# Kernel optimization log

Hardware: AMD Instinct MI355X
Metric: run time of the kernel (lower is better)

## Reference

```python
import jax, jax.numpy as jnp
import numpy as np


def setup_inputs() -> dict:
    key = jax.random.key(0)
    k1, k2 = jax.random.split(key)
    z_e_x = jax.random.normal(k1, (4096, 16, 128), dtype=jnp.float32)
    codebook = jax.random.normal(k2, (1024, 128), dtype=jnp.float32)
    return {"z_e_x": z_e_x, "codebook": codebook}


def reference(z_e_x, codebook):
    # VQStraightThrough.forward: nearest-codebook quantization in fp32.
    B, N, C = z_e_x.shape
    x = z_e_x.astype(jnp.float32).reshape(B * N, C)          # [BN, C]
    cb = codebook.astype(jnp.float32)                        # [K, C]
    inputs_sq = jnp.sum(x * x, axis=1, keepdims=True)        # [BN, 1]
    codebook_sq = jnp.sum(cb * cb, axis=1)                   # [K]
    l2_dis = inputs_sq + codebook_sq - 2.0 * (x @ cb.T)      # [BN, K]
    flat_idx = jnp.argmin(l2_dis, axis=1)                    # [BN] int
    min_vals = jnp.min(l2_dis, axis=1)                       # [BN]
    idx = flat_idx.reshape(B, N)
    distances = min_vals.reshape(B, N).astype(z_e_x.dtype)
    codes = cb[flat_idx].reshape(B, N, C).astype(z_e_x.dtype)  # gather
    return codes, flat_idx, idx, distances
```

## Files before the change

kernel.cpp:

```cpp
#include <hip/hip_runtime.h>
#include <math.h>
#include <stdint.h>

#define C        128
#define KCODES   1024
#define TPB      256
#define ROWS_PB  128
#define NCHUNK   64
#define NCHUNKS  (KCODES / NCHUNK)
#define BSTRIDE  272
#define BHALF    (NCHUNK * BSTRIDE)
#define BUFBYTES (2 * BHALF)
#define EPS_TRIG 0.25f

typedef __attribute__((ext_vector_type(8))) short bf16x8_t;
typedef __attribute__((ext_vector_type(4))) float f32x4_t;

static __device__ __forceinline__ uint32_t bf16_rne(float f) {
    uint32_t u = __float_as_uint(f);
    return (u + 0x7FFFu + ((u >> 16) & 1u)) >> 16;
}
static __device__ __forceinline__ float bf16_hi_f(float f) {
    return __uint_as_float(bf16_rne(f) << 16);
}

__global__ void cb_prep_kernel(const float* __restrict__ cb,
                               uint16_t* __restrict__ cbh,
                               uint16_t* __restrict__ cbl,
                               float* __restrict__ cbsq) {
    const int i = blockIdx.x * blockDim.x + threadIdx.x;
    if (i < KCODES * C) {
        float f = cb[i];
        uint32_t h = bf16_rne(f);
        float lo = f - __uint_as_float(h << 16);
        cbh[i] = (uint16_t)h;
        cbl[i] = (uint16_t)bf16_rne(lo);
    }
    if (i < KCODES) {
        const float4* cp = (const float4*)(cb + (size_t)i * C);
        float sx = 0.f, sy = 0.f, sz = 0.f, sw = 0.f;
        #pragma unroll
        for (int j = 0; j < C / 4; ++j) {
            float4 v = cp[j];
            sx += v.x * v.x; sy += v.y * v.y;
            sz += v.z * v.z; sw += v.w * v.w;
        }
        cbsq[i] = (sx + sy) + (sz + sw);
    }
}

#define SLOTS(OP) OP(0,0) OP(0,1) OP(0,2) OP(0,3) OP(1,0) OP(1,1) OP(1,2) OP(1,3)
#define MFMA_BF16 __builtin_amdgcn_mfma_f32_16x16x32_bf16

__global__ __launch_bounds__(TPB, 2)
void vq_mfma_kernel(const float* __restrict__ x,
                    const float* __restrict__ cb,
                    const uint16_t* __restrict__ cbh,
                    const uint16_t* __restrict__ cbl,
                    const float* __restrict__ cq,
                    float* __restrict__ out_codes,
                    float* __restrict__ out_fidx,
                    float* __restrict__ out_idx,
                    float* __restrict__ out_dist,
                    int rows)
{
    __shared__ __align__(16) uint8_t s_buf[2 * BUFBYTES];
    __shared__ float s_cq[2][NCHUNK];
    __shared__ float s_v1[ROWS_PB], s_v2[ROWS_PB];
    __shared__ int   s_k1[ROWS_PB], s_k2[ROWS_PB];

    const int t    = threadIdx.x;
    const int lane = t & 63;
    const int w    = t >> 6;
    const int ln   = lane & 15;
    const int quad = lane >> 4;
    const int rowblock = blockIdx.x * ROWS_PB;

    const uint4* cbh4 = (const uint4*)cbh;
    const uint4* cbl4 = (const uint4*)cbl;

    uint4 rh0, rh1, rh2, rh3, rl0, rl1, rl2, rl3;
    float cqr = 0.f;

#define STAGE_LOAD(chn) { \
    const size_t gb = (size_t)(chn) * (NCHUNK * 16); \
    rh0 = cbh4[gb + t + 0 * TPB]; rh1 = cbh4[gb + t + 1 * TPB]; \
    rh2 = cbh4[gb + t + 2 * TPB]; rh3 = cbh4[gb + t + 3 * TPB]; \
    rl0 = cbl4[gb + t + 0 * TPB]; rl1 = cbl4[gb + t + 1 * TPB]; \
    rl2 = cbl4[gb + t + 2 * TPB]; rl3 = cbl4[gb + t + 3 * TPB]; \
    if (t < NCHUNK) cqr = cq[(chn) * NCHUNK + t]; }

#define STAGE_WRITE(bi) { \
    uint8_t* sb = s_buf + (bi) * BUFBYTES; \
    { int uid = t + 0 * TPB; uint8_t* p = sb + (uid >> 4) * BSTRIDE + (uid & 15) * 16; \
      *(uint4*)p = rh0; *(uint4*)(p + BHALF) = rl0; } \
    { int uid = t + 1 * TPB; uint8_t* p = sb + (uid >> 4) * BSTRIDE + (uid & 15) * 16; \
      *(uint4*)p = rh1; *(uint4*)(p + BHALF) = rl1; } \
    { int uid = t + 2 * TPB; uint8_t* p = sb + (uid >> 4) * BSTRIDE + (uid & 15) * 16; \
      *(uint4*)p = rh2; *(uint4*)(p + BHALF) = rl2; } \
    { int uid = t + 3 * TPB; uint8_t* p = sb + (uid >> 4) * BSTRIDE + (uid & 15) * 16; \
      *(uint4*)p = rh3; *(uint4*)(p + BHALF) = rl3; } \
    if (t < NCHUNK) s_cq[bi][t] = cqr; }

    STAGE_LOAD(0);

    #pragma unroll 4
    for (int i = 0; i < 16; ++i) {
        int fid = t + i * TPB;
        int row = fid >> 5;
        int kq  = fid & 31;
        int grow = rowblock + row;
        grow = grow < rows ? grow : rows - 1;
        float4 v = ((const float4*)x)[(size_t)grow * 32 + kq];
        uint32_t p0 = bf16_rne(v.x) | (bf16_rne(v.y) << 16);
        uint32_t p1 = bf16_rne(v.z) | (bf16_rne(v.w) << 16);
        *(uint2*)(s_buf + row * BSTRIDE + kq * 8) = make_uint2(p0, p1);
    }
    __syncthreads();

    const int arow0 = (w * 32 + ln) * BSTRIDE;
    const int arow1 = (w * 32 + 16 + ln) * BSTRIDE;
    bf16x8_t ah00, ah01, ah02, ah03, ah10, ah11, ah12, ah13;
    ah00 = *(const bf16x8_t*)(s_buf + arow0 + 0 * 64 + quad * 16);
    ah01 = *(const bf16x8_t*)(s_buf + arow0 + 1 * 64 + quad * 16);
    ah02 = *(const bf16x8_t*)(s_buf + arow0 + 2 * 64 + quad * 16);
    ah03 = *(const bf16x8_t*)(s_buf + arow0 + 3 * 64 + quad * 16);
    ah10 = *(const bf16x8_t*)(s_buf + arow1 + 0 * 64 + quad * 16);
    ah11 = *(const bf16x8_t*)(s_buf + arow1 + 1 * 64 + quad * 16);
    ah12 = *(const bf16x8_t*)(s_buf + arow1 + 2 * 64 + quad * 16);
    ah13 = *(const bf16x8_t*)(s_buf + arow1 + 3 * 64 + quad * 16);
    __syncthreads();

    #pragma unroll 4
    for (int i = 0; i < 16; ++i) {
        int fid = t + i * TPB;
        int row = fid >> 5;
        int kq  = fid & 31;
        int grow = rowblock + row;
        grow = grow < rows ? grow : rows - 1;
        float4 v = ((const float4*)x)[(size_t)grow * 32 + kq];
        uint32_t p0 = bf16_rne(v.x - bf16_hi_f(v.x)) | (bf16_rne(v.y - bf16_hi_f(v.y)) << 16);
        uint32_t p1 = bf16_rne(v.z - bf16_hi_f(v.z)) | (bf16_rne(v.w - bf16_hi_f(v.w)) << 16);
        *(uint2*)(s_buf + row * BSTRIDE + kq * 8) = make_uint2(p0, p1);
    }
    __syncthreads();

    bf16x8_t al00, al01, al02, al03, al10, al11, al12, al13;
    al00 = *(const bf16x8_t*)(s_buf + arow0 + 0 * 64 + quad * 16);
    al01 = *(const bf16x8_t*)(s_buf + arow0 + 1 * 64 + quad * 16);
    al02 = *(const bf16x8_t*)(s_buf + arow0 + 2 * 64 + quad * 16);
    al03 = *(const bf16x8_t*)(s_buf + arow0 + 3 * 64 + quad * 16);
    al10 = *(const bf16x8_t*)(s_buf + arow1 + 0 * 64 + quad * 16);
    al11 = *(const bf16x8_t*)(s_buf + arow1 + 1 * 64 + quad * 16);
    al12 = *(const bf16x8_t*)(s_buf + arow1 + 2 * 64 + quad * 16);
    al13 = *(const bf16x8_t*)(s_buf + arow1 + 3 * 64 + quad * 16);
    __syncthreads();

    STAGE_WRITE(0);
    __syncthreads();

#define DECL(g,r) float v1_##g##r = INFINITY, v2_##g##r = INFINITY; int k1_##g##r = 0, k2_##g##r = 0;
    SLOTS(DECL)
#undef DECL

    #pragma unroll 1
    for (int chn = 0; chn < NCHUNKS; ++chn) {
        const int buf   = chn & 1;
        const int kbase = chn * NCHUNK;

        if (chn + 1 < NCHUNKS) STAGE_LOAD(chn + 1);

        const uint8_t* bbase = s_buf + buf * BUFBYTES + (size_t)ln * BSTRIDE + quad * 16;
        #pragma unroll
        for (int ct = 0; ct < 4; ++ct) {
            const uint8_t* bh_p = bbase + (size_t)ct * 16 * BSTRIDE;
            const uint8_t* bl_p = bh_p + BHALF;
            f32x4_t acc0 = {0.f, 0.f, 0.f, 0.f};
            f32x4_t acc1 = {0.f, 0.f, 0.f, 0.f};
#define KSTEP(kk) { \
            bf16x8_t bh = *(const bf16x8_t*)(bh_p + kk * 64); \
            bf16x8_t bl = *(const bf16x8_t*)(bl_p + kk * 64); \
            acc0 = MFMA_BF16(ah0##kk, bh, acc0, 0, 0, 0); \
            acc0 = MFMA_BF16(al0##kk, bh, acc0, 0, 0, 0); \
            acc0 = MFMA_BF16(ah0##kk, bl, acc0, 0, 0, 0); \
            acc1 = MFMA_BF16(ah1##kk, bh, acc1, 0, 0, 0); \
            acc1 = MFMA_BF16(al1##kk, bh, acc1, 0, 0, 0); \
            acc1 = MFMA_BF16(ah1##kk, bl, acc1, 0, 0, 0); }
            KSTEP(0) KSTEP(1) KSTEP(2) KSTEP(3)
#undef KSTEP
            const float cqv = s_cq[buf][ct * 16 + ln];
            const int   kc  = kbase + ct * 16 + ln;
#define UPD(g,r) { \
            float s_ = fmaf(-2.0f, (g ? acc1 : acc0)[r], cqv); \
            bool c1_ = s_ < v1_##g##r; \
            bool c2_ = s_ < v2_##g##r; \
            v2_##g##r = c1_ ? v1_##g##r : (c2_ ? s_ : v2_##g##r); \
            k2_##g##r = c1_ ? k1_##g##r : (c2_ ? kc : k2_##g##r); \
            v1_##g##r = c1_ ? s_ : v1_##g##r; \
            k1_##g##r = c1_ ? kc : k1_##g##r; }
            SLOTS(UPD)
#undef UPD
        }

        if (chn + 1 < NCHUNKS) STAGE_WRITE(buf ^ 1);
        __syncthreads();
    }

    for (int m_ = 1; m_ <= 8; m_ <<= 1) {
#define MRG(g,r) { \
        float ov1 = __shfl_xor(v1_##g##r, m_, 16); int ok1 = __shfl_xor(k1_##g##r, m_, 16); \
        float ov2 = __shfl_xor(v2_##g##r, m_, 16); int ok2 = __shfl_xor(k2_##g##r, m_, 16); \
        if (ov1 < v1_##g##r || (ov1 == v1_##g##r && ok1 < k1_##g##r)) { \
            if (v1_##g##r < ov2 || (v1_##g##r == ov2 && k1_##g##r < ok2)) { v2_##g##r = v1_##g##r; k2_##g##r = k1_##g##r; } \
            else { v2_##g##r = ov2; k2_##g##r = ok2; } \
            v1_##g##r = ov1; k1_##g##r = ok1; \
        } else if (ov1 < v2_##g##r || (ov1 == v2_##g##r && ok1 < k2_##g##r)) { \
            v2_##g##r = ov1; k2_##g##r = ok1; \
        } }
        SLOTS(MRG)
#undef MRG
    }
    if (ln == 0) {
#define WRT(g,r) { int rloc = w * 32 + g * 16 + quad * 4 + r; \
        s_v1[rloc] = v1_##g##r; s_v2[rloc] = v2_##g##r; \
        s_k1[rloc] = k1_##g##r; s_k2[rloc] = k2_##g##r; }
        SLOTS(WRT)
#undef WRT
    }
    __syncthreads();

    if (t < ROWS_PB) {
        int rowg = rowblock + t;
        const bool valid = rowg < rows;
        rowg = valid ? rowg : rows - 1;
        float v1 = s_v1[t], v2 = s_v2[t];
        int k1 = s_k1[t], k2 = s_k2[t];
        const float* xr = x + (size_t)rowg * C;

        float sx = 0.f, sy = 0.f, sz = 0.f, sw = 0.f;
        {
            const float4* xp = (const float4*)xr;
            #pragma unroll
            for (int i = 0; i < C / 4; ++i) {
                float4 v = xp[i];
                sx += v.x * v.x; sy += v.y * v.y;
                sz += v.z * v.z; sw += v.w * v.w;
            }
        }
        const float rs = (sx + sy) + (sz + sw);

        bool switched = false;
        double qwin = 0.0;
        if (v2 - v1 < EPS_TRIG) {
            const float* c1p = cb + (size_t)k1 * C;
            const float* c2p = cb + (size_t)k2 * C;
            double dot1 = 0.0, cq1 = 0.0, dot2 = 0.0, cq2 = 0.0;
            #pragma unroll 8
            for (int c = 0; c < C; ++c) {
                const double xc  = (double)xr[c];
                const double cv1 = (double)c1p[c];
                const double cv2 = (double)c2p[c];
                dot1 += xc * cv1;  cq1 += cv1 * cv1;
                dot2 += xc * cv2;  cq2 += cv2 * cv2;
            }
            const double q1 = cq1 - 2.0 * dot1;
            const double q2 = cq2 - 2.0 * dot2;
            if (q2 < q1 || (q2 == q1 && k2 < k1)) { k1 = k2; switched = true; qwin = q2; }
        }

        const float* c1p = cb + (size_t)k1 * C;
        float a = 0.f;
        #pragma unroll 16
        for (int c = 0; c < C; ++c) a = fmaf(xr[c], c1p[c], a);
        float d = (rs + cq[k1]) - 2.f * a;
        if (switched) d = (float)((double)rs + qwin);

        if (valid) {
            out_fidx[rowg] = (float)k1;
            out_idx[rowg]  = (float)k1;
            out_dist[rowg] = d;
        }
        s_k1[t] = k1;
    }
    __syncthreads();

    {
        const int r    = t >> 1;
        const int half = t & 1;
        const int rowg = rowblock + r;
        if (rowg < rows) {
            const int k1 = s_k1[r];
            const float4* src = (const float4*)(cb + (size_t)k1 * C) + half * 16;
            float4*       dst = (float4*)(out_codes + (size_t)rowg * C) + half * 16;
            #pragma unroll
            for (int i = 0; i < 16; ++i) dst[i] = src[i];
        }
    }
#undef STAGE_LOAD
#undef STAGE_WRITE
}

__global__ __launch_bounds__(TPB, 1)
void vq_nearest_fallback(const float* __restrict__ x,
                         const float* __restrict__ cb,
                         float* __restrict__ out_codes,
                         float* __restrict__ out_fidx,
                         float* __restrict__ out_idx,
                         float* __restrict__ out_dist,
                         int rows)
{
    __shared__ float s_cbsq[KCODES];
    const int t = threadIdx.x;
    for (int k = t; k < KCODES; k += TPB) {
        const float4* cp = (const float4*)(cb + (size_t)k * C);
        float sx = 0.f, sy = 0.f, sz = 0.f, sw = 0.f;
        #pragma unroll
        for (int i = 0; i < C / 4; ++i) {
            float4 v = cp[i];
            sx += v.x * v.x; sy += v.y * v.y; sz += v.z * v.z; sw += v.w * v.w;
        }
        s_cbsq[k] = (sx + sy) + (sz + sw);
    }
    __syncthreads();
    const int row = blockIdx.x * TPB + t;
    if (row >= rows) return;
    float xr[C];
    {
        const float4* xp = (const float4*)(x + (size_t)row * C);
        #pragma unroll
        for (int i = 0; i < C / 4; ++i) {
            float4 v = xp[i];
            xr[4*i+0] = v.x; xr[4*i+1] = v.y; xr[4*i+2] = v.z; xr[4*i+3] = v.w;
        }
    }
    float rs;
    {
        float sx = 0.f, sy = 0.f, sz = 0.f, sw = 0.f;
        #pragma unroll
        for (int i = 0; i < C / 4; ++i) {
            sx += xr[4*i+0]*xr[4*i+0]; sy += xr[4*i+1]*xr[4*i+1];
            sz += xr[4*i+2]*xr[4*i+2]; sw += xr[4*i+3]*xr[4*i+3];
        }
        rs = (sx + sy) + (sz + sw);
    }
    float v1 = INFINITY, v2 = INFINITY; int k1 = 0, k2 = 0;
    #pragma unroll 1
    for (int k0 = 0; k0 < KCODES; k0 += 4) {
        const float* c0 = cb + (size_t)k0 * C;
        float a0 = 0.f, a1 = 0.f, a2 = 0.f, a3 = 0.f;
        #pragma unroll
        for (int c = 0; c < C; ++c) {
            const float xc = xr[c];
            a0 = fmaf(xc, c0[c], a0);
            a1 = fmaf(xc, c0[C + c], a1);
            a2 = fmaf(xc, c0[2*C + c], a2);
            a3 = fmaf(xc, c0[3*C + c], a3);
        }
        const float d0 = (rs + s_cbsq[k0+0]) - 2.f * a0;
        const float d1 = (rs + s_cbsq[k0+1]) - 2.f * a1;
        const float d2 = (rs + s_cbsq[k0+2]) - 2.f * a2;
        const float d3 = (rs + s_cbsq[k0+3]) - 2.f * a3;
        #define UPDF(dv, ki)                                                 \
            if ((dv) < v1)      { v2 = v1; k2 = k1; v1 = (dv); k1 = (ki); } \
            else if ((dv) < v2) { v2 = (dv); k2 = (ki); }
        UPDF(d0, k0+0); UPDF(d1, k0+1); UPDF(d2, k0+2); UPDF(d3, k0+3);
        #undef UPDF
    }
    if (v2 - v1 < 0.125f) {
        const float* c1p = cb + (size_t)k1 * C;
        const float* c2p = cb + (size_t)k2 * C;
        double dot1 = 0.0, cq1 = 0.0, dot2 = 0.0, cq2 = 0.0;
        #pragma unroll 8
        for (int c = 0; c < C; ++c) {
            const double xc = (double)xr[c];
            const double cv1 = (double)c1p[c];
            const double cv2 = (double)c2p[c];
            dot1 += xc * cv1; cq1 += cv1 * cv1;
            dot2 += xc * cv2; cq2 += cv2 * cv2;
        }
        const double q1 = cq1 - 2.0 * dot1;
        const double q2 = cq2 - 2.0 * dot2;
        if (q2 < q1 || (q2 == q1 && k2 < k1)) { k1 = k2; v1 = (float)((double)rs + q2); }
    }
    {
        const float4* src = (const float4*)(cb + (size_t)k1 * C);
        float4* dst = (float4*)(out_codes + (size_t)row * C);
        #pragma unroll
        for (int i = 0; i < C / 4; ++i) dst[i] = src[i];
        out_fidx[row] = (float)k1;
        out_idx[row]  = (float)k1;
        out_dist[row] = v1;
    }
}

extern "C" void kernel_launch(void* const* d_in, const int* in_sizes, int n_in,
                              void* d_out, int out_size, void* d_ws, size_t ws_size,
                              hipStream_t stream) {
    const float* x  = (const float*)d_in[0];
    const float* cb = (const float*)d_in[1];
    const int rows = in_sizes[0] / C;

    float* out       = (float*)d_out;
    float* out_codes = out;
    float* out_fidx  = out + (size_t)rows * C;
    float* out_idx   = out_fidx + rows;
    float* out_dist  = out_idx + rows;

    const size_t cbh_off = 0;
    const size_t cbl_off = (size_t)KCODES * C * sizeof(uint16_t);
    const size_t cq_off  = cbl_off * 2;
    const size_t need    = cq_off + KCODES * sizeof(float);

    if (ws_size >= need) {
        uint16_t* cbh = (uint16_t*)((char*)d_ws + cbh_off);
        uint16_t* cbl = (uint16_t*)((char*)d_ws + cbl_off);
        float*    cq  = (float*)((char*)d_ws + cq_off);

        cb_prep_kernel<<<(KCODES * C + TPB - 1) / TPB, TPB, 0, stream>>>(cb, cbh, cbl, cq);

        const int grid = (rows + ROWS_PB - 1) / ROWS_PB;
        vq_mfma_kernel<<<grid, TPB, 0, stream>>>(x, cb, cbh, cbl, cq,
                                                 out_codes, out_fidx, out_idx,
                                                 out_dist, rows);
    } else {
        const int rowblocks = (rows + TPB - 1) / TPB;
        vq_nearest_fallback<<<rowblocks, TPB, 0, stream>>>(x, cb, out_codes, out_fidx,
                                                           out_idx, out_dist, rows);
    }
}
```

Measured before the change: 164.6 us.

## Load codebook MFMA operands directly from global into registers with ping-pong prefetch

Removes the shared-memory double-buffered codebook staging and its per-chunk barriers. Each wave now reads its bf16 hi/lo codebook fragments and codebook norms straight from global memory (L2/L1 cached) into registers, software-pipelined across two register sets. This cuts LDS traffic, LDS footprint and __syncthreads. In exchange, every wave issues redundant global loads of the same codebook data and needs more VGPRs for the prefetch sets.

Measured after the change: 238.9 us. 1.45x slower.

```diff
diff --git a/kernel.cpp b/kernel.cpp
--- a/kernel.cpp
+++ b/kernel.cpp
@@ -6,11 +6,8 @@
 #define KCODES   1024
 #define TPB      256
 #define ROWS_PB  128
-#define NCHUNK   64
-#define NCHUNKS  (KCODES / NCHUNK)
+#define NKT      (KCODES / 16)
 #define BSTRIDE  272
-#define BHALF    (NCHUNK * BSTRIDE)
-#define BUFBYTES (2 * BHALF)
 #define EPS_TRIG 0.25f
 
 typedef __attribute__((ext_vector_type(8))) short bf16x8_t;
@@ -64,8 +61,7 @@
                     float* __restrict__ out_dist,
                     int rows)
 {
-    __shared__ __align__(16) uint8_t s_buf[2 * BUFBYTES];
-    __shared__ float s_cq[2][NCHUNK];
+    __shared__ __align__(16) uint8_t s_buf[ROWS_PB * BSTRIDE];
     __shared__ float s_v1[ROWS_PB], s_v2[ROWS_PB];
     __shared__ int   s_k1[ROWS_PB], s_k2[ROWS_PB];
 
@@ -75,34 +71,6 @@
     const int ln   = lane & 15;
     const int quad = lane >> 4;
     const int rowblock = blockIdx.x * ROWS_PB;
-
-    const uint4* cbh4 = (const uint4*)cbh;
-    const uint4* cbl4 = (const uint4*)cbl;
-
-    uint4 rh0, rh1, rh2, rh3, rl0, rl1, rl2, rl3;
-    float cqr = 0.f;
-
-#define STAGE_LOAD(chn) { \
-    const size_t gb = (size_t)(chn) * (NCHUNK * 16); \
-    rh0 = cbh4[gb + t + 0 * TPB]; rh1 = cbh4[gb + t + 1 * TPB]; \
-    rh2 = cbh4[gb + t + 2 * TPB]; rh3 = cbh4[gb + t + 3 * TPB]; \
-    rl0 = cbl4[gb + t + 0 * TPB]; rl1 = cbl4[gb + t + 1 * TPB]; \
-    rl2 = cbl4[gb + t + 2 * TPB]; rl3 = cbl4[gb + t + 3 * TPB]; \
-    if (t < NCHUNK) cqr = cq[(chn) * NCHUNK + t]; }
-
-#define STAGE_WRITE(bi) { \
-    uint8_t* sb = s_buf + (bi) * BUFBYTES; \
-    { int uid = t + 0 * TPB; uint8_t* p = sb + (uid >> 4) * BSTRIDE + (uid & 15) * 16; \
-      *(uint4*)p = rh0; *(uint4*)(p + BHALF) = rl0; } \
-    { int uid = t + 1 * TPB; uint8_t* p = sb + (uid >> 4) * BSTRIDE + (uid & 15) * 16; \
-      *(uint4*)p = rh1; *(uint4*)(p + BHALF) = rl1; } \
-    { int uid = t + 2 * TPB; uint8_t* p = sb + (uid >> 4) * BSTRIDE + (uid & 15) * 16; \
-      *(uint4*)p = rh2; *(uint4*)(p + BHALF) = rl2; } \
-    { int uid = t + 3 * TPB; uint8_t* p = sb + (uid >> 4) * BSTRIDE + (uid & 15) * 16; \
-      *(uint4*)p = rh3; *(uint4*)(p + BHALF) = rl3; } \
-    if (t < NCHUNK) s_cq[bi][t] = cqr; }
-
-    STAGE_LOAD(0);
 
     #pragma unroll 4
     for (int i = 0; i < 16; ++i) {
@@ -156,55 +124,82 @@
     al13 = *(const bf16x8_t*)(s_buf + arow1 + 3 * 64 + quad * 16);
     __syncthreads();
 
-    STAGE_WRITE(0);
-    __syncthreads();
-
 #define DECL(g,r) float v1_##g##r = INFINITY, v2_##g##r = INFINITY; int k1_##g##r = 0, k2_##g##r = 0;
     SLOTS(DECL)
 #undef DECL
 
+    const uint8_t* bh_lane = (const uint8_t*)cbh + (size_t)ln * 256 + quad * 16;
+    const uint8_t* bl_lane = (const uint8_t*)cbl + (size_t)ln * 256 + quad * 16;
+
+#define DECL_B(S) bf16x8_t bh##S##0, bh##S##1, bh##S##2, bh##S##3, \
+                           bl##S##0, bl##S##1, bl##S##2, bl##S##3; float cqv##S;
+
+#define LOAD_B(S, kt) { \
+    const uint8_t* hp = bh_lane + (size_t)(kt) * 4096; \
+    const uint8_t* lp = bl_lane + (size_t)(kt) * 4096; \
+    bh##S##0 = *(const bf16x8_t*)(hp + 0 * 64); \
+    bh##S##1 = *(const bf16x8_t*)(hp + 1 * 64); \
+    bh##S##2 = *(const bf16x8_t*)(hp + 2 * 64); \
+    bh##S##3 = *(const bf16x8_t*)(hp + 3 * 64); \
+    bl##S##0 = *(const bf16x8_t*)(lp + 0 * 64); \
+    bl##S##1 = *(const bf16x8_t*)(lp + 1 * 64); \
+    bl##S##2 = *(const bf16x8_t*)(lp + 2 * 64); \
+    bl##S##3 = *(const bf16x8_t*)(lp + 3 * 64); \
+    cqv##S = cq[(kt) * 16 + ln]; }
+
+#define COMPUTE_B(S, kt) { \
+    f32x4_t acc0 = {0.f, 0.f, 0.f, 0.f}; \
+    f32x4_t acc1 = {0.f, 0.f, 0.f, 0.f}; \
+    acc0 = MFMA_BF16(ah00, bh##S##0, acc0, 0, 0, 0); \
+    acc0 = MFMA_BF16(al00, bh##S##0, acc0, 0, 0, 0); \
+    acc0 = MFMA_BF16(ah00, bl##S##0, acc0, 0, 0, 0); \
+    acc1 = MFMA_BF16(ah10, bh##S##0, acc1, 0, 0, 0); \
+    acc1 = MFMA_BF16(al10, bh##S##0, acc1, 0, 0, 0); \
+    acc1 = MFMA_BF16(ah10, bl##S##0, acc1, 0, 0, 0); \
+    acc0 = MFMA_BF16(ah01, bh##S##1, acc0, 0, 0, 0); \
+    acc0 = MFMA_BF16(al01, bh##S##1, acc0, 0, 0, 0); \
+    acc0 = MFMA_BF16(ah01, bl##S##1, acc0, 0, 0, 0); \
+    acc1 = MFMA_BF16(ah11, bh##S##1, acc1, 0, 0, 0); \
+    acc1 = MFMA_BF16(al11, bh##S##1, acc1, 0, 0, 0); \
+    acc1 = MFMA_BF16(ah11, bl##S##1, acc1, 0, 0, 0); \
+    acc0 = MFMA_BF16(ah02, bh##S##2, acc0, 0, 0, 0); \
+    acc0 = MFMA_BF16(al02, bh##S##2, acc0, 0, 0, 0); \
+    acc0 = MFMA_BF16(ah02, bl##S##2, acc0, 0, 0, 0); \
+    acc1 = MFMA_BF16(ah12, bh##S##2, acc1, 0, 0, 0); \
+    acc1 = MFMA_BF16(al12, bh##S##2, acc1, 0, 0, 0); \
+    acc1 = MFMA_BF16(ah12, bl##S##2, acc1, 0, 0, 0); \
+    acc0 = MFMA_BF16(ah03, bh##S##3, acc0, 0, 0, 0); \
+    acc0 = MFMA_BF16(al03, bh##S##3, acc0, 0, 0, 0); \
+    acc0 = MFMA_BF16(ah03, bl##S##3, acc0, 0, 0, 0); \
+    acc1 = MFMA_BF16(ah13, bh##S##3, acc1, 0, 0, 0); \
+    acc1 = MFMA_BF16(al13, bh##S##3, acc1, 0, 0, 0); \
+    acc1 = MFMA_BF16(ah13, bl##S##3, acc1, 0, 0, 0); \
+    const float cqv = cqv##S; \
+    const int   kc  = (kt) * 16 + ln; \
+    SLOTS(UPD) }
+
+#define UPD(g,r) { \
+    float s_ = fmaf(-2.0f, (g ? acc1 : acc0)[r], cqv); \
+    bool c1_ = s_ < v1_##g##r; \
+    bool c2_ = s_ < v2_##g##r; \
+    v2_##g##r = c1_ ? v1_##g##r : (c2_ ? s_ : v2_##g##r); \
+    k2_##g##r = c1_ ? k1_##g##r : (c2_ ? kc : k2_##g##r); \
+    v1_##g##r = c1_ ? s_ : v1_##g##r; \
+    k1_##g##r = c1_ ? kc : k1_##g##r; }
+
+    DECL_B(A) DECL_B(B)
+    LOAD_B(A, 0);
     #pragma unroll 1
-    for (int chn = 0; chn < NCHUNKS; ++chn) {
-        const int buf   = chn & 1;
-        const int kbase = chn * NCHUNK;
-
-        if (chn + 1 < NCHUNKS) STAGE_LOAD(chn + 1);
-
-        const uint8_t* bbase = s_buf + buf * BUFBYTES + (size_t)ln * BSTRIDE + quad * 16;
-        #pragma unroll
-        for (int ct = 0; ct < 4; ++ct) {
-            const uint8_t* bh_p = bbase + (size_t)ct * 16 * BSTRIDE;
-            const uint8_t* bl_p = bh_p + BHALF;
-            f32x4_t acc0 = {0.f, 0.f, 0.f, 0.f};
-            f32x4_t acc1 = {0.f, 0.f, 0.f, 0.f};
-#define KSTEP(kk) { \
-            bf16x8_t bh = *(const bf16x8_t*)(bh_p + kk * 64); \
-            bf16x8_t bl = *(const bf16x8_t*)(bl_p + kk * 64); \
-            acc0 = MFMA_BF16(ah0##kk, bh, acc0, 0, 0, 0); \
-            acc0 = MFMA_BF16(al0##kk, bh, acc0, 0, 0, 0); \
-            acc0 = MFMA_BF16(ah0##kk, bl, acc0, 0, 0, 0); \
-            acc1 = MFMA_BF16(ah1##kk, bh, acc1, 0, 0, 0); \
-            acc1 = MFMA_BF16(al1##kk, bh, acc1, 0, 0, 0); \
-            acc1 = MFMA_BF16(ah1##kk, bl, acc1, 0, 0, 0); }
-            KSTEP(0) KSTEP(1) KSTEP(2) KSTEP(3)
-#undef KSTEP
-            const float cqv = s_cq[buf][ct * 16 + ln];
-            const int   kc  = kbase + ct * 16 + ln;
-#define UPD(g,r) { \
-            float s_ = fmaf(-2.0f, (g ? acc1 : acc0)[r], cqv); \
-            bool c1_ = s_ < v1_##g##r; \
-            bool c2_ = s_ < v2_##g##r; \
-            v2_##g##r = c1_ ? v1_##g##r : (c2_ ? s_ : v2_##g##r); \
-            k2_##g##r = c1_ ? k1_##g##r : (c2_ ? kc : k2_##g##r); \
-            v1_##g##r = c1_ ? s_ : v1_##g##r; \
-            k1_##g##r = c1_ ? kc : k1_##g##r; }
-            SLOTS(UPD)
+    for (int kt = 0; kt < NKT; kt += 2) {
+        LOAD_B(B, kt + 1);
+        COMPUTE_B(A, kt);
+        if (kt + 2 < NKT) LOAD_B(A, kt + 2);
+        COMPUTE_B(B, kt + 1);
+    }
 #undef UPD
-        }
-
-        if (chn + 1 < NCHUNKS) STAGE_WRITE(buf ^ 1);
-        __syncthreads();
-    }
+#undef COMPUTE_B
+#undef LOAD_B
+#undef DECL_B
 
     for (int m_ = 1; m_ <= 8; m_ <<= 1) {
 #define MRG(g,r) { \
@@ -296,8 +291,6 @@
             for (int i = 0; i < 16; ++i) dst[i] = src[i];
         }
     }
-#undef STAGE_LOAD
-#undef STAGE_WRITE
 }
 
 __global__ __launch_bounds__(TPB, 1)
```
